# Kernel tuning notes

Hardware: AMD Instinct MI355X
Metric: run time of the kernel (lower is better)

The kernel has to match this reference:

```python
import jax, jax.numpy as jnp
import numpy as np

D_MODEL = 1024
NUM_HEADS = 16
SEQ_LEN = 2048
BATCH = 2
THETA = 10000.0


def apply_rope(x, positions, theta):
    # x: [..., seq, d_k]; positions: [seq]
    dk = x.shape[-1]
    half = dk // 2
    k = jnp.arange(half, dtype=jnp.float32)
    inv_freq = theta ** (-2.0 * k / dk)                 # [half]
    ang = positions.astype(jnp.float32)[:, None] * inv_freq  # [seq, half]
    cos, sin = jnp.cos(ang), jnp.sin(ang)
    xe = x[..., 0::2]   # even members of adjacent pairs
    xo = x[..., 1::2]
    out_e = cos * xe - sin * xo
    out_o = sin * xe + cos * xo
    # interleave pairs back: [..., seq, half, 2] -> [..., seq, dk]
    return jnp.stack([out_e, out_o], axis=-1).reshape(x.shape)


def setup_inputs() -> dict:
    key = jax.random.key(0)
    kx, kq, kk, kv, ko = jax.random.split(key, 5)
    sig = 1.0 / np.sqrt(D_MODEL)
    def tn(k):
        return jnp.clip(jax.random.normal(k, (D_MODEL, D_MODEL), jnp.float32), -3.0, 3.0) * sig
    return {
        "x": jax.random.normal(kx, (BATCH, SEQ_LEN, D_MODEL), jnp.float32),
        "q_proj_weight": tn(kq),
        "k_proj_weight": tn(kk),
        "v_proj_weight": tn(kv),
        "o_proj_weight": tn(ko),
        "token_positions": jnp.arange(SEQ_LEN, dtype=jnp.int32),
    }


def reference(x, q_proj_weight, k_proj_weight, v_proj_weight, o_proj_weight, token_positions):
    h = NUM_HEADS
    d = x.shape[-1]
    dh = d // h
    seq = x.shape[-2]
    Wq = q_proj_weight.reshape(h, dh, d)
    Wk = k_proj_weight.reshape(h, dh, d)
    Wv = v_proj_weight.reshape(h, dh, d)
    Q = jnp.einsum('bsd,hed->bhse', x, Wq)
    K = jnp.einsum('bsd,hed->bhse', x, Wk)
    V = jnp.einsum('bsd,hed->bhse', x, Wv)
    Q = apply_rope(Q, token_positions, THETA)
    K = apply_rope(K, token_positions, THETA)
    scores = jnp.einsum('bhqe,bhke->bhqk', Q, K) / jnp.sqrt(jnp.float32(dh))
    mask = jnp.tril(jnp.ones((seq, seq), dtype=bool))
    scores = jnp.where(mask, scores, -jnp.inf)
    probs = jax.nn.softmax(scores, axis=-1)
    att = jnp.einsum('bhqk,bhke->bhqe', probs, V)       # [b, h, s, dh]
    att = att.transpose(0, 2, 1, 3).reshape(x.shape[0], seq, d)  # concat heads
    return jnp.einsum('bsh,dh->bsd', att, o_proj_weight)
```

## Files before the change

kernel.cpp:

```cpp
#include <hip/hip_runtime.h>
#include <hip/hip_bf16.h>
#include <cstdint>
#include <cstddef>

#define DEV static __device__ __forceinline__

typedef __bf16 bf16x8 __attribute__((ext_vector_type(8)));
typedef float f32x4 __attribute__((ext_vector_type(4)));
typedef unsigned short u16;

static constexpr int BATCH = 2, SEQ = 2048, DM = 1024, NH = 16, DH = 64;
static constexpr int Kdim = 1024;
static constexpr int BS = BATCH * SEQ;

DEV u16 f2b(float f) {
  uint32_t u = __builtin_bit_cast(uint32_t, f);
  u += 0x7FFFu + ((u >> 16) & 1u);
  return (u16)(u >> 16);
}

DEV void gload_lds16(const void* g, void* l) {
  __builtin_amdgcn_global_load_lds((const __attribute__((address_space(1))) void*)g,
                                   (__attribute__((address_space(3))) void*)l, 16, 0, 0);
}

DEV void plswap32(uint32_t& a, uint32_t& b) {
  asm("v_permlane32_swap_b32 %0, %1" : "+v"(a), "+v"(b));
}
DEV void plswap16(uint32_t& a, uint32_t& b) {
  asm("v_permlane16_swap_b32 %0, %1" : "+v"(a), "+v"(b));
}

__global__ __launch_bounds__(256) void cast_all(const float* __restrict__ x,
    const float* __restrict__ wq, const float* __restrict__ wk,
    const float* __restrict__ wv, const float* __restrict__ wo,
    const int* __restrict__ pos,
    u16* __restrict__ xb, u16* __restrict__ wqb, u16* __restrict__ wkb,
    u16* __restrict__ wvb, u16* __restrict__ wob, float2* __restrict__ tab) {
  const int NX = (BATCH * SEQ * DM) / 4;
  const int NW = (DM * DM) / 4;
  const int NT = SEQ * 32;
  int i = blockIdx.x * blockDim.x + threadIdx.x;
  const int stride = gridDim.x * blockDim.x;
  for (; i < NX + 4 * NW + NT; i += stride) {
    if (i < NX + 4 * NW) {
      const float* src; u16* dst; int off;
      if (i < NX) { src = x; dst = xb; off = i; }
      else {
        const int j = i - NX, seg = j >> 18;
        off = j & (NW - 1);
        src = seg == 0 ? wq : seg == 1 ? wk : seg == 2 ? wv : wo;
        dst = seg == 0 ? wqb : seg == 1 ? wkb : seg == 2 ? wvb : wob;
      }
      float4 v = ((const float4*)src)[off];
      ushort4 o;
      o.x = f2b(v.x); o.y = f2b(v.y); o.z = f2b(v.z); o.w = f2b(v.w);
      ((ushort4*)dst)[off] = o;
    } else {
      const int t = i - NX - 4 * NW;
      const int s = t >> 5, j = t & 31;
      const float ang = (float)pos[s] * exp2f((float)j * -0.4152410118609203f);
      float sn, cs;
      sincosf(ang, &sn, &cs);
      tab[t] = make_float2(cs, sn);
    }
  }
}

template <int BN, bool OUTF32, int ROPE>
DEV void gemm_core(const u16* __restrict__ A, const u16* __restrict__ Bm,
                   void* __restrict__ Cout, int ldC, int m0, int n0,
                   u16* __restrict__ As, u16* __restrict__ Bs,
                   const float2* __restrict__ tab) {
  const int tid = threadIdx.x;
  const int lane = tid & 63, wid = tid >> 6;
  const int wr = (wid >> 1) * 64, wc = (wid & 1) * (BN / 2);
  const int frow = lane & 15, fgrp = lane >> 4;
  constexpr int NF = BN / 32;
  constexpr int BSZ = BN * 32;
  constexpr int NK = Kdim / 32;
  f32x4 acc[4][NF] = {};

  const int c0 = tid, c1 = tid + 256;
  const int ra0 = c0 >> 2, sa0 = (c0 & 3) ^ ((ra0 >> 1) & 3);
  const int ra1 = c1 >> 2, sa1 = (c1 & 3) ^ ((ra1 >> 1) & 3);
  const size_t gA0 = (size_t)(m0 + ra0) * Kdim + sa0 * 8;
  const size_t gA1 = (size_t)(m0 + ra1) * Kdim + sa1 * 8;
  const size_t gB0 = (size_t)(n0 + ra0) * Kdim + sa0 * 8;
  const size_t gB1 = (size_t)(n0 + ra1) * Kdim + sa1 * 8;

#define GSTAGE(bufi, kofs)                                                      \
  do {                                                                          \
    gload_lds16(A + gA0 + (kofs), As + (bufi) * 4096 + wid * 512);              \
    gload_lds16(A + gA1 + (kofs), As + (bufi) * 4096 + wid * 512 + 2048);       \
    gload_lds16(Bm + gB0 + (kofs), Bs + (bufi) * BSZ + wid * 512);              \
    if (BN == 128)                                                              \
      gload_lds16(Bm + gB1 + (kofs), Bs + (bufi) * BSZ + wid * 512 + 2048);     \
  } while (0)

  GSTAGE(0, 0);
  for (int kt = 0; kt < NK; ++kt) {
    const int buf = kt & 1;
    if (kt + 1 < NK) {
      GSTAGE((kt + 1) & 1, (kt + 1) * 32);
      if (BN == 128) asm volatile("s_waitcnt vmcnt(4)" ::: "memory");
      else           asm volatile("s_waitcnt vmcnt(3)" ::: "memory");
    } else {
      asm volatile("s_waitcnt vmcnt(0)" ::: "memory");
    }
    __builtin_amdgcn_s_barrier();

    bf16x8 af[4], bfr[NF];
#pragma unroll
    for (int i = 0; i < 4; ++i) {
      const int ra = wr + i * 16 + frow;
      af[i] = *(const bf16x8*)((const char*)(As + buf * 4096) + ra * 64 +
                               ((fgrp ^ ((ra >> 1) & 3)) * 16));
    }
#pragma unroll
    for (int f = 0; f < NF; ++f) {
      const int rb = wc + f * 16 + frow;
      bfr[f] = *(const bf16x8*)((const char*)(Bs + buf * BSZ) + rb * 64 +
                                ((fgrp ^ ((rb >> 1) & 3)) * 16));
    }
#pragma unroll
    for (int mi = 0; mi < 4; ++mi)
#pragma unroll
      for (int f = 0; f < NF; ++f)
        acc[mi][f] = __builtin_amdgcn_mfma_f32_16x16x32_bf16(af[mi], bfr[f], acc[mi][f], 0, 0, 0);

    __builtin_amdgcn_s_barrier();
  }
#undef GSTAGE

  const int colb = n0 + wc + frow;
  const int rowb = m0 + wr + fgrp * 4;
  if (ROPE) {
#pragma unroll
    for (int mi = 0; mi < 4; ++mi)
#pragma unroll
      for (int f = 0; f < NF; ++f) {
        const int col = colb + f * 16;
        const int j = (col & 63) >> 1;
#pragma unroll
        for (int r = 0; r < 4; ++r) {
          const float v = acc[mi][f][r];
          const float partner = __shfl_xor(v, 1);
          const int row = rowb + mi * 16 + r;
          const float2 cs_ = tab[(row & (SEQ - 1)) * 32 + j];
          float outv = (col & 1) ? fmaf(cs_.y, partner, cs_.x * v)
                                 : fmaf(cs_.x, v, -cs_.y * partner);
          if (ROPE == 1) outv *= 0.18033688011112043f;
          acc[mi][f][r] = outv;
        }
      }
  }
#pragma unroll
  for (int mi = 0; mi < 4; ++mi)
#pragma unroll
    for (int f = 0; f < NF; ++f)
#pragma unroll
      for (int r = 0; r < 4; ++r) {
        const int row = rowb + mi * 16 + r;
        const int col = colb + f * 16;
        const float v = acc[mi][f][r];
        if (OUTF32) ((float*)Cout)[(size_t)row * ldC + col] = v;
        else        ((u16*)Cout)[(size_t)row * ldC + col] = f2b(v);
      }
}

__global__ __launch_bounds__(256) void gemm_qkvt(const u16* __restrict__ xb,
    const u16* __restrict__ wq, const u16* __restrict__ wk, const u16* __restrict__ wv,
    u16* __restrict__ Qb, u16* __restrict__ Kb, u16* __restrict__ Vtb,
    const float2* __restrict__ tab) {
  __shared__ u16 As[2][4096], Bs[2][2048];
  const int f = blockIdx.x, z = blockIdx.z;
  const int xcd = f & 7, j = f >> 3;
  if (z == 0) {
    const int m0 = (xcd * 4 + (j >> 4)) * 128, n0 = (j & 15) * 64;
    gemm_core<64, false, 1>(xb, wq, Qb, DM, m0, n0, &As[0][0], &Bs[0][0], tab);
  } else if (z == 1) {
    const int m0 = (xcd * 4 + (j >> 4)) * 128, n0 = (j & 15) * 64;
    gemm_core<64, false, 2>(xb, wk, Kb, DM, m0, n0, &As[0][0], &Bs[0][0], tab);
  } else {
    const int m0 = xcd * 128, n0 = j * 64;
    gemm_core<64, false, 0>(wv, xb, Vtb, BS, m0, n0, &As[0][0], &Bs[0][0], nullptr);
  }
}

__global__ __launch_bounds__(256) void gemm_o(const u16* __restrict__ attb,
                                              const u16* __restrict__ wob,
                                              float* __restrict__ out) {
  __shared__ u16 As[2][4096], Bs[2][2048];
  const int f = blockIdx.x;
  const int xcd = f & 7, k = f >> 3;
  const int grp = xcd * 8 + (k >> 3);
  const int m0 = (grp >> 1) * 128;
  const int n0 = ((grp & 1) * 8 + (k & 7)) * 64;
  gemm_core<64, true, 0>(attb, wob, out, DM, m0, n0, &As[0][0], &Bs[0][0], nullptr);
}

__global__ __launch_bounds__(256, 2) void attn_kernel(const u16* __restrict__ Qb,
                                                      const u16* __restrict__ Kb,
                                                      const u16* __restrict__ Vtb,
                                                      u16* __restrict__ attb) {
  __shared__ __align__(16) unsigned char SM[73728];
  u16* Qs = (u16*)(SM + 65536);
  float* Of = (float*)SM;
  float* Ld = (float*)(SM + 65536);

  const int tid = threadIdx.x, lane = tid & 63, wid = tid >> 6;
  const int flat = (int)blockIdx.x + 16 * (int)blockIdx.y;
  const int orig = (flat & 7) * 64 + (flat >> 3);
  const int xq = orig & 15;
  const int bh = orig >> 4;
  const int b = bh >> 4, h = bh & 15;
  const size_t base_bh = ((size_t)b * SEQ) * DM + h * DH;
  const int frow = lane & 15, fgrp = lane >> 4;
  const int w32 = wid * 32;
  const int swz = (frow & 7) << 4;

  const u16* Ksrcs[4];
  const u16* Vsrcs[4];
#pragma unroll
  for (int i = 0; i < 4; ++i) {
    const int c = tid + i * 256;
    const int rk = c >> 3, s8 = (c & 7) ^ (rk & 7);
    Ksrcs[i] = Kb + base_bh + (size_t)rk * DM + s8 * 8;
    const int rv = c >> 4, s16 = (c & 15) ^ (rv & 7);
    Vsrcs[i] = Vtb + (size_t)(h * DH + rv) * BS + (size_t)b * SEQ + s16 * 8;
  }
  const int cq0 = tid, cq1 = tid + 256;
  const int rq0 = cq0 >> 3, sq0 = (cq0 & 7) ^ (rq0 & 7);
  const int rq1 = cq1 >> 3, sq1 = (cq1 & 7) ^ (rq1 & 7);

#pragma unroll 1
  for (int phase = 0; phase < 2; ++phase) {
    const int qt = phase ? xq : 31 - xq;
    const int q0 = qt * 64;
    const int nkv = (qt >> 1) + 1;

    gload_lds16(Qb + base_bh + (size_t)(q0 + rq0) * DM + sq0 * 8, (char*)SM + 65536 + tid * 16);
    gload_lds16(Qb + base_bh + (size_t)(q0 + rq1) * DM + sq1 * 8, (char*)SM + 69632 + tid * 16);
#pragma unroll
    for (int i = 0; i < 4; ++i) {
      gload_lds16(Ksrcs[i], (char*)SM + wid * 1024 + i * 4096);
      gload_lds16(Vsrcs[i], (char*)SM + 32768 + wid * 1024 + i * 4096);
    }
    __syncthreads();

    bf16x8 qf[4][2];
#pragma unroll
    for (int qs = 0; qs < 4; ++qs)
#pragma unroll
      for (int ks = 0; ks < 2; ++ks) {
        const int byte = ((qs * 16 + frow) * 128 + ks * 64 + fgrp * 16) ^ swz;
        qf[qs][ks] = *(const bf16x8*)((const char*)Qs + byte);
      }

    f32x4 accO[4][4] = {};
    float l_lane[4] = {0.f, 0.f, 0.f, 0.f};

    for (int kt = 0; kt < nkv; ++kt) {
      const char* Kc = (const char*)SM + (kt & 1) * 16384;
      const char* Vc = (const char*)SM + 32768 + (kt & 1) * 16384;
      if (kt + 1 < nkv) {
        const size_t kvn = (size_t)(kt + 1) * 128;
        const int nb = (kt + 1) & 1;
#pragma unroll
        for (int i = 0; i < 4; ++i) {
          gload_lds16(Ksrcs[i] + kvn * DM, (char*)SM + nb * 16384 + wid * 1024 + i * 4096);
          gload_lds16(Vsrcs[i] + kvn, (char*)SM + 32768 + nb * 16384 + wid * 1024 + i * 4096);
        }
      }

      f32x4 sc[4][2] = {};
      __builtin_amdgcn_s_setprio(1);
#pragma unroll
      for (int tc = 0; tc < 2; ++tc)
#pragma unroll
        for (int ks = 0; ks < 2; ++ks) {
          const int byte = ((w32 + tc * 16 + frow) * 128 + ks * 64 + fgrp * 16) ^ swz;
          const bf16x8 kf = *(const bf16x8*)(Kc + byte);
#pragma unroll
          for (int qs = 0; qs < 4; ++qs)
            sc[qs][tc] = __builtin_amdgcn_mfma_f32_16x16x32_bf16(kf, qf[qs][ks], sc[qs][tc], 0, 0, 0);
        }
      __builtin_amdgcn_s_setprio(0);

      if (kt == nkv - 1) {
        const int kv0 = kt * 128;
#pragma unroll
        for (int qs = 0; qs < 4; ++qs)
#pragma unroll
          for (int tc = 0; tc < 2; ++tc)
#pragma unroll
            for (int r = 0; r < 4; ++r)
              if (kv0 + w32 + tc * 16 + fgrp * 4 + r > q0 + qs * 16 + frow)
                sc[qs][tc][r] = -1e30f;
      }

      bf16x8 pf[4];
#pragma unroll
      for (int qs = 0; qs < 4; ++qs) {
        const float p00 = exp2f(sc[qs][0][0]), p01 = exp2f(sc[qs][0][1]);
        const float p02 = exp2f(sc[qs][0][2]), p03 = exp2f(sc[qs][0][3]);
        const float p10 = exp2f(sc[qs][1][0]), p11 = exp2f(sc[qs][1][1]);
        const float p12 = exp2f(sc[qs][1][2]), p13 = exp2f(sc[qs][1][3]);
        l_lane[qs] += ((p00 + p01) + (p02 + p03)) + ((p10 + p11) + (p12 + p13));
        union { __bf16 bb[2]; uint32_t uu; } c00, c01, c10, c11;
        c00.bb[0] = (__bf16)p00; c00.bb[1] = (__bf16)p01;
        c01.bb[0] = (__bf16)p02; c01.bb[1] = (__bf16)p03;
        c10.bb[0] = (__bf16)p10; c10.bb[1] = (__bf16)p11;
        c11.bb[0] = (__bf16)p12; c11.bb[1] = (__bf16)p13;
        uint32_t a0 = c00.uu, a1 = c01.uu, b0 = c10.uu, b1 = c11.uu;
        plswap32(a0, b0); plswap16(a0, b0);
        plswap32(a1, b1); plswap16(a1, b1);
        union { uint32_t w[4]; bf16x8 v; } pk;
        pk.w[0] = a0; pk.w[1] = a1; pk.w[2] = b0; pk.w[3] = b1;
        pf[qs] = pk.v;
      }

      __builtin_amdgcn_s_setprio(1);
#pragma unroll
      for (int te = 0; te < 4; ++te) {
        const int byte = ((te * 16 + frow) * 256 + wid * 64 + fgrp * 16) ^ swz;
        const bf16x8 vf = *(const bf16x8*)(Vc + byte);
#pragma unroll
        for (int qs = 0; qs < 4; ++qs)
          accO[qs][te] = __builtin_amdgcn_mfma_f32_16x16x32_bf16(pf[qs], vf, accO[qs][te], 0, 0, 0);
      }
      __builtin_amdgcn_s_setprio(0);
      __syncthreads();
    }

    float* myOf = Of + wid * 4096;
#pragma unroll
    for (int qs = 0; qs < 4; ++qs)
#pragma unroll
      for (int te = 0; te < 4; ++te)
#pragma unroll
        for (int r = 0; r < 4; ++r)
          myOf[(qs * 16 + fgrp * 4 + r) * 64 + te * 16 + frow] = accO[qs][te][r];
#pragma unroll
    for (int qs = 0; qs < 4; ++qs) {
      l_lane[qs] += __shfl_xor(l_lane[qs], 16);
      l_lane[qs] += __shfl_xor(l_lane[qs], 32);
    }
    if (fgrp == 0) {
#pragma unroll
      for (int qs = 0; qs < 4; ++qs) Ld[wid * 64 + qs * 16 + frow] = l_lane[qs];
    }
    __syncthreads();

    {
      const int qlb = wid * 16 + fgrp * 4;
#pragma unroll
      for (int i = 0; i < 4; ++i) {
        const int ql = qlb + i;
        f32x4 s = {};
#pragma unroll
        for (int wv = 0; wv < 4; ++wv) {
          const f32x4 t = *(const f32x4*)(Of + wv * 4096 + ql * 64 + frow * 4);
          s += t;
        }
        const float lq = ((Ld[ql] + Ld[64 + ql]) + (Ld[128 + ql] + Ld[192 + ql]));
        const float inv = 1.0f / lq;
        ushort4 o;
        o.x = f2b(s[0] * inv); o.y = f2b(s[1] * inv);
        o.z = f2b(s[2] * inv); o.w = f2b(s[3] * inv);
        *(ushort4*)(attb + base_bh + (size_t)(q0 + ql) * DM + frow * 4) = o;
      }
    }
    __syncthreads();
  }
}

extern "C" void kernel_launch(void* const* d_in, const int* in_sizes, int n_in,
                              void* d_out, int out_size, void* d_ws, size_t ws_size,
                              hipStream_t stream) {
  const float* x  = (const float*)d_in[0];
  const float* wq = (const float*)d_in[1];
  const float* wk = (const float*)d_in[2];
  const float* wv = (const float*)d_in[3];
  const float* wo = (const float*)d_in[4];
  const int* pos  = (const int*)d_in[5];
  float* out = (float*)d_out;
  (void)in_sizes; (void)n_in; (void)out_size; (void)ws_size;

  char* ws = (char*)d_ws;
  const size_t MB = 1024 * 1024;
  u16* xb   = (u16*)(ws);
  u16* wqb  = (u16*)(ws + 8 * MB);
  u16* wkb  = (u16*)(ws + 10 * MB);
  u16* wvb  = (u16*)(ws + 12 * MB);
  u16* wob  = (u16*)(ws + 14 * MB);
  u16* Qb   = (u16*)(ws + 16 * MB);
  u16* Kb   = (u16*)(ws + 24 * MB);
  u16* Vtb  = (u16*)(ws + 32 * MB);
  u16* attb = (u16*)(ws + 40 * MB);
  float2* tab = (float2*)(ws + 40 * MB);

  cast_all<<<2048, 256, 0, stream>>>(x, wq, wk, wv, wo, pos, xb, wqb, wkb, wvb, wob, tab);
  gemm_qkvt<<<dim3(512, 1, 3), 256, 0, stream>>>(xb, wqb, wkb, wvb, Qb, Kb, Vtb, tab);
  attn_kernel<<<dim3(16, 32), 256, 0, stream>>>(Qb, Kb, Vtb, attb);
  gemm_o<<<512, 256, 0, stream>>>(attb, wob, out);
}
```

Before: 115.6 us.

## Split attention block into 8 waves across query halves and KV quarters

The attention kernel now launches 512 threads per block instead of 256. Waves are split two ways: two groups over query rows (32 rows each) and four over KV columns. This halves each wave's accumulator and score registers and raises the launch-bounds occupancy target to 4. It adds a cross-wave reduction over the four KV-split partials per query half, and the 72KB shared buffer may still cap how many blocks fit per CU.

```diff
diff --git a/kernel.cpp b/kernel.cpp
--- a/kernel.cpp
+++ b/kernel.cpp
@@ -200,16 +200,16 @@
   gemm_core<64, true, 0>(attb, wob, out, DM, m0, n0, &As[0][0], &Bs[0][0], nullptr);
 }
 
-__global__ __launch_bounds__(256, 2) void attn_kernel(const u16* __restrict__ Qb,
+__global__ __launch_bounds__(512, 4) void attn_kernel(const u16* __restrict__ Qb,
                                                       const u16* __restrict__ Kb,
                                                       const u16* __restrict__ Vtb,
                                                       u16* __restrict__ attb) {
   __shared__ __align__(16) unsigned char SM[73728];
-  u16* Qs = (u16*)(SM + 65536);
   float* Of = (float*)SM;
   float* Ld = (float*)(SM + 65536);
 
   const int tid = threadIdx.x, lane = tid & 63, wid = tid >> 6;
+  const int qh = wid >> 2, kq = wid & 3;
   const int flat = (int)blockIdx.x + 16 * (int)blockIdx.y;
   const int orig = (flat & 7) * 64 + (flat >> 3);
   const int xq = orig & 15;
@@ -217,22 +217,20 @@
   const int b = bh >> 4, h = bh & 15;
   const size_t base_bh = ((size_t)b * SEQ) * DM + h * DH;
   const int frow = lane & 15, fgrp = lane >> 4;
-  const int w32 = wid * 32;
+  const int kq32 = kq * 32;
   const int swz = (frow & 7) << 4;
 
-  const u16* Ksrcs[4];
-  const u16* Vsrcs[4];
-#pragma unroll
-  for (int i = 0; i < 4; ++i) {
-    const int c = tid + i * 256;
+  const u16* Ksrcs[2];
+  const u16* Vsrcs[2];
+#pragma unroll
+  for (int i = 0; i < 2; ++i) {
+    const int c = tid + i * 512;
     const int rk = c >> 3, s8 = (c & 7) ^ (rk & 7);
     Ksrcs[i] = Kb + base_bh + (size_t)rk * DM + s8 * 8;
     const int rv = c >> 4, s16 = (c & 15) ^ (rv & 7);
     Vsrcs[i] = Vtb + (size_t)(h * DH + rv) * BS + (size_t)b * SEQ + s16 * 8;
   }
-  const int cq0 = tid, cq1 = tid + 256;
-  const int rq0 = cq0 >> 3, sq0 = (cq0 & 7) ^ (rq0 & 7);
-  const int rq1 = cq1 >> 3, sq1 = (cq1 & 7) ^ (rq1 & 7);
+  const int rq = tid >> 3, sq = (tid & 7) ^ (rq & 7);
 
 #pragma unroll 1
   for (int phase = 0; phase < 2; ++phase) {
@@ -240,26 +238,25 @@
     const int q0 = qt * 64;
     const int nkv = (qt >> 1) + 1;
 
-    gload_lds16(Qb + base_bh + (size_t)(q0 + rq0) * DM + sq0 * 8, (char*)SM + 65536 + tid * 16);
-    gload_lds16(Qb + base_bh + (size_t)(q0 + rq1) * DM + sq1 * 8, (char*)SM + 69632 + tid * 16);
-#pragma unroll
-    for (int i = 0; i < 4; ++i) {
-      gload_lds16(Ksrcs[i], (char*)SM + wid * 1024 + i * 4096);
-      gload_lds16(Vsrcs[i], (char*)SM + 32768 + wid * 1024 + i * 4096);
+    gload_lds16(Qb + base_bh + (size_t)(q0 + rq) * DM + sq * 8, (char*)SM + 65536 + tid * 16);
+#pragma unroll
+    for (int i = 0; i < 2; ++i) {
+      gload_lds16(Ksrcs[i], (char*)SM + i * 8192 + tid * 16);
+      gload_lds16(Vsrcs[i], (char*)SM + 32768 + i * 8192 + tid * 16);
     }
     __syncthreads();
 
-    bf16x8 qf[4][2];
-#pragma unroll
-    for (int qs = 0; qs < 4; ++qs)
+    bf16x8 qf[2][2];
+#pragma unroll
+    for (int qs = 0; qs < 2; ++qs)
 #pragma unroll
       for (int ks = 0; ks < 2; ++ks) {
-        const int byte = ((qs * 16 + frow) * 128 + ks * 64 + fgrp * 16) ^ swz;
-        qf[qs][ks] = *(const bf16x8*)((const char*)Qs + byte);
-      }
-
-    f32x4 accO[4][4] = {};
-    float l_lane[4] = {0.f, 0.f, 0.f, 0.f};
+        const int byte = ((qh * 32 + qs * 16 + frow) * 128 + ks * 64 + fgrp * 16) ^ swz;
+        qf[qs][ks] = *(const bf16x8*)((const char*)SM + 65536 + byte);
+      }
+
+    f32x4 accO[2][4] = {};
+    float l_lane[2] = {0.f, 0.f};
 
     for (int kt = 0; kt < nkv; ++kt) {
       const char* Kc = (const char*)SM + (kt & 1) * 16384;
@@ -268,22 +265,22 @@
         const size_t kvn = (size_t)(kt + 1) * 128;
         const int nb = (kt + 1) & 1;
 #pragma unroll
-        for (int i = 0; i < 4; ++i) {
-          gload_lds16(Ksrcs[i] + kvn * DM, (char*)SM + nb * 16384 + wid * 1024 + i * 4096);
-          gload_lds16(Vsrcs[i] + kvn, (char*)SM + 32768 + nb * 16384 + wid * 1024 + i * 4096);
+        for (int i = 0; i < 2; ++i) {
+          gload_lds16(Ksrcs[i] + kvn * DM, (char*)SM + nb * 16384 + i * 8192 + tid * 16);
+          gload_lds16(Vsrcs[i] + kvn, (char*)SM + 32768 + nb * 16384 + i * 8192 + tid * 16);
         }
       }
 
-      f32x4 sc[4][2] = {};
+      f32x4 sc[2][2] = {};
       __builtin_amdgcn_s_setprio(1);
 #pragma unroll
       for (int tc = 0; tc < 2; ++tc)
 #pragma unroll
         for (int ks = 0; ks < 2; ++ks) {
-          const int byte = ((w32 + tc * 16 + frow) * 128 + ks * 64 + fgrp * 16) ^ swz;
+          const int byte = ((kq32 + tc * 16 + frow) * 128 + ks * 64 + fgrp * 16) ^ swz;
           const bf16x8 kf = *(const bf16x8*)(Kc + byte);
 #pragma unroll
-          for (int qs = 0; qs < 4; ++qs)
+          for (int qs = 0; qs < 2; ++qs)
             sc[qs][tc] = __builtin_amdgcn_mfma_f32_16x16x32_bf16(kf, qf[qs][ks], sc[qs][tc], 0, 0, 0);
         }
       __builtin_amdgcn_s_setprio(0);
@@ -291,18 +288,18 @@
       if (kt == nkv - 1) {
         const int kv0 = kt * 128;
 #pragma unroll
-        for (int qs = 0; qs < 4; ++qs)
+        for (int qs = 0; qs < 2; ++qs)
 #pragma unroll
           for (int tc = 0; tc < 2; ++tc)
 #pragma unroll
             for (int r = 0; r < 4; ++r)
-              if (kv0 + w32 + tc * 16 + fgrp * 4 + r > q0 + qs * 16 + frow)
+              if (kv0 + kq32 + tc * 16 + fgrp * 4 + r > q0 + qh * 32 + qs * 16 + frow)
                 sc[qs][tc][r] = -1e30f;
       }
 
-      bf16x8 pf[4];
-#pragma unroll
-      for (int qs = 0; qs < 4; ++qs) {
+      bf16x8 pf[2];
+#pragma unroll
+      for (int qs = 0; qs < 2; ++qs) {
         const float p00 = exp2f(sc[qs][0][0]), p01 = exp2f(sc[qs][0][1]);
         const float p02 = exp2f(sc[qs][0][2]), p03 = exp2f(sc[qs][0][3]);
         const float p10 = exp2f(sc[qs][1][0]), p11 = exp2f(sc[qs][1][1]);
@@ -324,53 +321,51 @@
       __builtin_amdgcn_s_setprio(1);
 #pragma unroll
       for (int te = 0; te < 4; ++te) {
-        const int byte = ((te * 16 + frow) * 256 + wid * 64 + fgrp * 16) ^ swz;
+        const int byte = ((te * 16 + frow) * 256 + kq * 64 + fgrp * 16) ^ swz;
         const bf16x8 vf = *(const bf16x8*)(Vc + byte);
 #pragma unroll
-        for (int qs = 0; qs < 4; ++qs)
+        for (int qs = 0; qs < 2; ++qs)
           accO[qs][te] = __builtin_amdgcn_mfma_f32_16x16x32_bf16(pf[qs], vf, accO[qs][te], 0, 0, 0);
       }
       __builtin_amdgcn_s_setprio(0);
       __syncthreads();
     }
 
-    float* myOf = Of + wid * 4096;
-#pragma unroll
-    for (int qs = 0; qs < 4; ++qs)
+    float* myOf = Of + wid * 2048;
+#pragma unroll
+    for (int qs = 0; qs < 2; ++qs)
 #pragma unroll
       for (int te = 0; te < 4; ++te)
 #pragma unroll
         for (int r = 0; r < 4; ++r)
           myOf[(qs * 16 + fgrp * 4 + r) * 64 + te * 16 + frow] = accO[qs][te][r];
 #pragma unroll
-    for (int qs = 0; qs < 4; ++qs) {
+    for (int qs = 0; qs < 2; ++qs) {
       l_lane[qs] += __shfl_xor(l_lane[qs], 16);
       l_lane[qs] += __shfl_xor(l_lane[qs], 32);
     }
     if (fgrp == 0) {
 #pragma unroll
-      for (int qs = 0; qs < 4; ++qs) Ld[wid * 64 + qs * 16 + frow] = l_lane[qs];
+      for (int qs = 0; qs < 2; ++qs) Ld[wid * 32 + qs * 16 + frow] = l_lane[qs];
     }
     __syncthreads();
 
-    {
-      const int qlb = wid * 16 + fgrp * 4;
-#pragma unroll
-      for (int i = 0; i < 4; ++i) {
-        const int ql = qlb + i;
-        f32x4 s = {};
-#pragma unroll
-        for (int wv = 0; wv < 4; ++wv) {
-          const f32x4 t = *(const f32x4*)(Of + wv * 4096 + ql * 64 + frow * 4);
-          s += t;
-        }
-        const float lq = ((Ld[ql] + Ld[64 + ql]) + (Ld[128 + ql] + Ld[192 + ql]));
-        const float inv = 1.0f / lq;
-        ushort4 o;
-        o.x = f2b(s[0] * inv); o.y = f2b(s[1] * inv);
-        o.z = f2b(s[2] * inv); o.w = f2b(s[3] * inv);
-        *(ushort4*)(attb + base_bh + (size_t)(q0 + ql) * DM + frow * 4) = o;
-      }
+#pragma unroll
+    for (int ii = 0; ii < 2; ++ii) {
+      const int ql = wid * 8 + fgrp * 2 + ii;
+      const int hh = ql >> 5, qlh = ql & 31;
+      f32x4 s = {};
+      float lq = 0.f;
+#pragma unroll
+      for (int j = 0; j < 4; ++j) {
+        s += *(const f32x4*)(Of + (hh * 4 + j) * 2048 + qlh * 64 + frow * 4);
+        lq += Ld[(hh * 4 + j) * 32 + qlh];
+      }
+      const float inv = 1.0f / lq;
+      ushort4 o;
+      o.x = f2b(s[0] * inv); o.y = f2b(s[1] * inv);
+      o.z = f2b(s[2] * inv); o.w = f2b(s[3] * inv);
+      *(ushort4*)(attb + base_bh + (size_t)(q0 + ql) * DM + frow * 4) = o;
     }
     __syncthreads();
   }
@@ -403,6 +398,6 @@
 
   cast_all<<<2048, 256, 0, stream>>>(x, wq, wk, wv, wo, pos, xb, wqb, wkb, wvb, wob, tab);
   gemm_qkvt<<<dim3(512, 1, 3), 256, 0, stream>>>(xb, wqb, wkb, wvb, Qb, Kb, Vtb, tab);
-  attn_kernel<<<dim3(16, 32), 256, 0, stream>>>(Qb, Kb, Vtb, attb);
+  attn_kernel<<<dim3(16, 32), 512, 0, stream>>>(Qb, Kb, Vtb, attb);
   gemm_o<<<512, 256, 0, stream>>>(attb, wob, out);
 }
```

After: 117.0 us. About the same (+1.2%).
